# Optimization experiments

Hardware: AMD Instinct MI355X
Metric: run time of the kernel (lower is better)

Reference implementation:

```python
import jax, jax.numpy as jnp
import numpy as np

ALPHA = 1.0  # Student-t degrees of freedom (DEC default)


def setup_inputs() -> dict:
    key = jax.random.key(0)
    k1, k2 = jax.random.split(key)
    N, K, D = 32768, 1000, 1024
    h = jax.random.normal(k1, (N, D), dtype=jnp.float32)
    centroids = jax.random.normal(k2, (K, D), dtype=jnp.float32)
    return {"h": h, "centroids": centroids}


def reference(h, centroids):
    # squared pairwise L2 distance via the GEMM expansion:
    # ||h_i - mu_j||^2 = ||h_i||^2 + ||mu_j||^2 - 2 h_i . mu_j
    h_sq = jnp.sum(h * h, axis=1, keepdims=True)            # [N, 1]
    c_sq = jnp.sum(centroids * centroids, axis=1)           # [K]
    cross = jnp.einsum('nd,kd->nk', h, centroids)           # [N, K]
    d2 = jnp.maximum(h_sq + c_sq[None, :] - 2.0 * cross, 0.0)
    # Student-t kernel soft assignment (DEC):
    # q_ij = (1 + d2/alpha)^(-(alpha+1)/2) / sum_j'
    power = -(ALPHA + 1.0) / 2.0
    q = (1.0 + d2 / ALPHA) ** power                          # [N, K]
    q = q / jnp.sum(q, axis=1, keepdims=True)
    return q
```

## Files before the change

### kernel.cpp

```cpp
#include <hip/hip_runtime.h>


typedef unsigned short u16;
typedef __attribute__((ext_vector_type(8))) short bf16x8;
typedef __attribute__((ext_vector_type(4))) float f32x4;

#define N_ROWS 32768
#define K_CENT 1000
#define KP     1024
#define DDIM   1024

__device__ __forceinline__ u16 f2bf(float x) {
  unsigned u = __float_as_uint(x);
  u += 0x7fffu + ((u >> 16) & 1u);
  return (u16)(u >> 16);
}

__device__ __forceinline__ void gload_lds16(const u16* g, u16* s) {
  __builtin_amdgcn_global_load_lds((__attribute__((address_space(1))) void*)g,
                                   (__attribute__((address_space(3))) void*)s,
                                   16, 0, 0);
}


__global__ __launch_bounds__(256) void prep_h(const float* __restrict__ h,
                                              u16* __restrict__ hb,
                                              float* __restrict__ hsq,
                                              float* __restrict__ rowsum) {
  const int row = blockIdx.x;
  const int t = threadIdx.x;
  const float4 v = reinterpret_cast<const float4*>(h + (size_t)row * DDIM)[t];
  ushort4 b;
  b.x = f2bf(v.x); b.y = f2bf(v.y); b.z = f2bf(v.z); b.w = f2bf(v.w);
  reinterpret_cast<ushort4*>(hb + (size_t)row * DDIM)[t] = b;
  float ss = v.x * v.x + v.y * v.y + v.z * v.z + v.w * v.w;
#pragma unroll
  for (int m = 1; m < 64; m <<= 1) ss += __shfl_xor(ss, m);
  __shared__ float sbuf[4];
  if ((t & 63) == 0) sbuf[t >> 6] = ss;
  __syncthreads();
  if (t == 0) {
    hsq[row] = sbuf[0] + sbuf[1] + sbuf[2] + sbuf[3];
    rowsum[row] = 0.0f;
  }
}

__global__ __launch_bounds__(256) void prep_c(const float* __restrict__ c,
                                              u16* __restrict__ cb,
                                              float* __restrict__ csq) {
  const int row = blockIdx.x;
  const int t = threadIdx.x;
  if (row < K_CENT) {
    const float4 v = reinterpret_cast<const float4*>(c + (size_t)row * DDIM)[t];
    ushort4 b;
    b.x = f2bf(v.x); b.y = f2bf(v.y); b.z = f2bf(v.z); b.w = f2bf(v.w);
    reinterpret_cast<ushort4*>(cb + (size_t)row * DDIM)[t] = b;
    float ss = v.x * v.x + v.y * v.y + v.z * v.z + v.w * v.w;
#pragma unroll
    for (int m = 1; m < 64; m <<= 1) ss += __shfl_xor(ss, m);
    __shared__ float sbuf[4];
    if ((t & 63) == 0) sbuf[t >> 6] = ss;
    __syncthreads();
    if (t == 0) csq[row] = sbuf[0] + sbuf[1] + sbuf[2] + sbuf[3];
  } else {
    ushort4 z; z.x = z.y = z.z = z.w = 0;
    reinterpret_cast<ushort4*>(cb + (size_t)row * DDIM)[t] = z;
    if (t == 0) csq[row] = 1e30f;
  }
}


__device__ __forceinline__ void stage_tile(const u16* __restrict__ gA,
                                           const u16* __restrict__ gB,
                                           u16* sA, u16* sB,
                                           int w, int l, int k0) {
#pragma unroll
  for (int i = 0; i < 2; ++i) {
    const int c = w + i * 4;
    const int roff = c * 16 + (l >> 2);
    const int koff = (l & 3) * 8;
    const size_t go = (size_t)roff * DDIM + k0 + koff;
    gload_lds16(gA + go, sA + c * 512);
    gload_lds16(gB + go, sB + c * 512);
  }
}

__global__ __launch_bounds__(256) void gemm_q(const u16* __restrict__ hb,
                                              const u16* __restrict__ cb,
                                              const float* __restrict__ hsq,
                                              const float* __restrict__ csq,
                                              float* __restrict__ out,
                                              float* __restrict__ rowsum) {
  __shared__ u16 As[2][128 * 32];
  __shared__ u16 Bs[2][128 * 32];

  const int bid = blockIdx.x;
  const int swz = ((bid & 7) << 8) | (bid >> 3);
  const int bcol = swz & 7;
  const int brow = swz >> 3;

  const int t = threadIdx.x;
  const int w = t >> 6;
  const int l = t & 63;
  const int wr = w >> 1;
  const int wc = w & 1;

  const u16* gA = hb + (size_t)brow * 128 * DDIM;
  const u16* gB = cb + (size_t)bcol * 128 * DDIM;

  f32x4 acc[4][4] = {};

  stage_tile(gA, gB, &As[0][0], &Bs[0][0], w, l, 0);

  const int NT = DDIM / 32;
  for (int kt = 0; kt < NT; ++kt) {
    const int cur = kt & 1;
    __syncthreads();
    if (kt + 1 < NT)
      stage_tile(gA, gB, &As[cur ^ 1][0], &Bs[cur ^ 1][0], w, l, (kt + 1) * 32);

    bf16x8 aF[4], bF[4];
#pragma unroll
    for (int m = 0; m < 4; ++m) {
      aF[m] = *(const bf16x8*)&As[cur][(wr * 64 + m * 16 + (l & 15)) * 32 + (l >> 4) * 8];
      bF[m] = *(const bf16x8*)&Bs[cur][(wc * 64 + m * 16 + (l & 15)) * 32 + (l >> 4) * 8];
    }
#pragma unroll
    for (int m = 0; m < 4; ++m)
#pragma unroll
      for (int n = 0; n < 4; ++n)
        acc[m][n] = __builtin_amdgcn_mfma_f32_16x16x32_bf16(aF[m], bF[n], acc[m][n], 0, 0, 0);
  }

  const int gi0 = brow * 128 + wr * 64;
  const int gj0 = bcol * 128 + wc * 64;
  const int lr = (l >> 4) << 2;
  const int lc = l & 15;

#pragma unroll
  for (int m = 0; m < 4; ++m) {
    float hs[4];
#pragma unroll
    for (int r = 0; r < 4; ++r) hs[r] = hsq[gi0 + m * 16 + lr + r];
    float rs[4] = {0.f, 0.f, 0.f, 0.f};
#pragma unroll
    for (int n = 0; n < 4; ++n) {
      const int gj = gj0 + n * 16 + lc;
      const float cs = csq[gj];
#pragma unroll
      for (int r = 0; r < 4; ++r) {
        float d2 = hs[r] + cs - 2.0f * acc[m][n][r];
        d2 = fmaxf(d2, 0.0f);
        const float qv = 1.0f / (1.0f + d2);
        rs[r] += qv;
        if (gj < K_CENT)
          out[(size_t)(gi0 + m * 16 + lr + r) * K_CENT + gj] = qv;
      }
    }
#pragma unroll
    for (int r = 0; r < 4; ++r) {
      float v = rs[r];
      v += __shfl_xor(v, 1);
      v += __shfl_xor(v, 2);
      v += __shfl_xor(v, 4);
      v += __shfl_xor(v, 8);
      if (lc == 0) atomicAdd(&rowsum[gi0 + m * 16 + lr + r], v);
    }
  }
}


__global__ __launch_bounds__(256) void norm_k(float* __restrict__ out,
                                              const float* __restrict__ rowsum) {
  const int row = blockIdx.x;
  const int t = threadIdx.x;
  if (t < 250) {
    const float inv = 1.0f / rowsum[row];
    float4* p = reinterpret_cast<float4*>(out) + (size_t)row * 250 + t;
    float4 v = *p;
    v.x *= inv; v.y *= inv; v.z *= inv; v.w *= inv;
    *p = v;
  }
}


extern "C" void kernel_launch(void* const* d_in, const int* in_sizes, int n_in,
                              void* d_out, int out_size, void* d_ws, size_t ws_size,
                              hipStream_t stream) {
  const float* h   = (const float*)d_in[0];
  const float* cen = (const float*)d_in[1];
  float* out = (float*)d_out;
  char* ws = (char*)d_ws;

  u16*   cb     = (u16*)(ws);
  u16*   hb     = (u16*)(ws + 2097152);
  float* hsq    = (float*)(ws + 2097152 + 67108864);
  float* csq    = (float*)(ws + 2097152 + 67108864 + 131072);
  float* rowsum = (float*)(ws + 2097152 + 67108864 + 131072 + 4096);

  prep_c<<<KP, 256, 0, stream>>>(cen, cb, csq);
  prep_h<<<N_ROWS, 256, 0, stream>>>(h, hb, hsq, rowsum);
  gemm_q<<<(N_ROWS / 128) * (KP / 128), 256, 0, stream>>>(hb, cb, hsq, csq, out, rowsum);
  norm_k<<<N_ROWS, 256, 0, stream>>>(out, rowsum);
}
```

Measured before the change: 192.1 us.

## Enlarge GEMM tile to 256x256 with 4-stage LDS pipeline and swizzled layout

Moves the GEMM to 256x256 block tiles with 512 threads and 8 waves, each wave computing 128x64. A four-buffer LDS ring keeps three k-tiles in flight, with explicit vmcnt waits, barriers, and staging of the next tiles interleaved between MFMA groups. s_setprio is raised around the MFMA groups. An XOR swizzle on the LDS layout is meant to avoid bank conflicts. The goal is more data reuse per block and hiding of global-load latency. In exchange it uses much more LDS (128KB per block) and more accumulator registers, which lowers occupancy.

```diff
diff --git a/kernel.cpp b/kernel.cpp
--- a/kernel.cpp
+++ b/kernel.cpp
@@ -9,6 +9,7 @@
 #define K_CENT 1000
 #define KP     1024
 #define DDIM   1024
+#define NT     32
 
 __device__ __forceinline__ u16 f2bf(float x) {
   unsigned u = __float_as_uint(x);
@@ -70,75 +71,112 @@
 }
 
 
-__device__ __forceinline__ void stage_tile(const u16* __restrict__ gA,
-                                           const u16* __restrict__ gB,
-                                           u16* sA, u16* sB,
-                                           int w, int l, int k0) {
+__device__ __forceinline__ void stageA(const u16* __restrict__ gA, u16* sA,
+                                       int tid, int t) {
 #pragma unroll
   for (int i = 0; i < 2; ++i) {
-    const int c = w + i * 4;
-    const int roff = c * 16 + (l >> 2);
-    const int koff = (l & 3) * 8;
-    const size_t go = (size_t)roff * DDIM + k0 + koff;
-    gload_lds16(gA + go, sA + c * 512);
-    gload_lds16(gB + go, sB + c * 512);
-  }
-}
-
-__global__ __launch_bounds__(256) void gemm_q(const u16* __restrict__ hb,
-                                              const u16* __restrict__ cb,
-                                              const float* __restrict__ hsq,
-                                              const float* __restrict__ csq,
-                                              float* __restrict__ out,
-                                              float* __restrict__ rowsum) {
-  __shared__ u16 As[2][128 * 32];
-  __shared__ u16 Bs[2][128 * 32];
+    const int p = tid + i * 512;
+    const int g = p ^ ((p >> 3) & 7);
+    gload_lds16(gA + (size_t)(g >> 2) * DDIM + t * 32 + (g & 3) * 8,
+                sA + (((tid & ~63) + i * 512) << 3));
+  }
+}
+__device__ __forceinline__ void stageB(const u16* __restrict__ gB, u16* sB,
+                                       int tid, int t) {
+#pragma unroll
+  for (int i = 0; i < 2; ++i) {
+    const int p = tid + i * 512;
+    const int g = p ^ ((p >> 3) & 7);
+    gload_lds16(gB + (size_t)(g >> 2) * DDIM + t * 32 + (g & 3) * 8,
+                sB + (((tid & ~63) + i * 512) << 3));
+  }
+}
+
+__global__ __launch_bounds__(512, 2) void gemm_q(const u16* __restrict__ hb,
+                                                 const u16* __restrict__ cb,
+                                                 const float* __restrict__ hsq,
+                                                 const float* __restrict__ csq,
+                                                 float* __restrict__ out,
+                                                 float* __restrict__ rowsum) {
+  __shared__ u16 As[4][8192];
+  __shared__ u16 Bs[4][8192];
 
   const int bid = blockIdx.x;
-  const int swz = ((bid & 7) << 8) | (bid >> 3);
-  const int bcol = swz & 7;
-  const int brow = swz >> 3;
-
-  const int t = threadIdx.x;
-  const int w = t >> 6;
-  const int l = t & 63;
-  const int wr = w >> 1;
-  const int wc = w & 1;
-
-  const u16* gA = hb + (size_t)brow * 128 * DDIM;
-  const u16* gB = cb + (size_t)bcol * 128 * DDIM;
-
-  f32x4 acc[4][4] = {};
-
-  stage_tile(gA, gB, &As[0][0], &Bs[0][0], w, l, 0);
-
-  const int NT = DDIM / 32;
-  for (int kt = 0; kt < NT; ++kt) {
-    const int cur = kt & 1;
-    __syncthreads();
-    if (kt + 1 < NT)
-      stage_tile(gA, gB, &As[cur ^ 1][0], &Bs[cur ^ 1][0], w, l, (kt + 1) * 32);
-
-    bf16x8 aF[4], bF[4];
-#pragma unroll
-    for (int m = 0; m < 4; ++m) {
-      aF[m] = *(const bf16x8*)&As[cur][(wr * 64 + m * 16 + (l & 15)) * 32 + (l >> 4) * 8];
-      bF[m] = *(const bf16x8*)&Bs[cur][(wc * 64 + m * 16 + (l & 15)) * 32 + (l >> 4) * 8];
-    }
-#pragma unroll
-    for (int m = 0; m < 4; ++m)
-#pragma unroll
-      for (int n = 0; n < 4; ++n)
-        acc[m][n] = __builtin_amdgcn_mfma_f32_16x16x32_bf16(aF[m], bF[n], acc[m][n], 0, 0, 0);
-  }
-
-  const int gi0 = brow * 128 + wr * 64;
-  const int gj0 = bcol * 128 + wc * 64;
+  const int swz = ((bid & 7) << 6) | (bid >> 3);
+  const int bcol = swz & 3;
+  const int brow = swz >> 2;
+
+  const int tid = threadIdx.x;
+  const int w = tid >> 6;
+  const int l = tid & 63;
+  const int wm = w >> 2;
+  const int wn = w & 3;
+
+  const u16* gA = hb + (size_t)brow * 256 * DDIM;
+  const u16* gB = cb + (size_t)bcol * 256 * DDIM;
+
+  stageA(gA, As[0], tid, 0); stageB(gB, Bs[0], tid, 0);
+  stageA(gA, As[1], tid, 1); stageB(gB, Bs[1], tid, 1);
+  stageA(gA, As[2], tid, 2); stageB(gB, Bs[2], tid, 2);
+
+  int aOff[8], bOff[4];
+#pragma unroll
+  for (int m = 0; m < 8; ++m) {
+    const int row = wm * 128 + m * 16 + (l & 15);
+    const int g = (row << 2) | (l >> 4);
+    aOff[m] = (g ^ ((g >> 3) & 7)) << 3;
+  }
+#pragma unroll
+  for (int n = 0; n < 4; ++n) {
+    const int row = wn * 64 + n * 16 + (l & 15);
+    const int g = (row << 2) | (l >> 4);
+    bOff[n] = (g ^ ((g >> 3) & 7)) << 3;
+  }
+
+  f32x4 acc[8][4] = {};
+
+#define KTILE_BODY(T, VM)                                                      \
+  {                                                                            \
+    const int s_ = (T) & 3, ns_ = ((T) + 3) & 3;                               \
+    asm volatile("s_waitcnt vmcnt(" #VM ")" ::: "memory");                     \
+    __builtin_amdgcn_s_barrier();                                              \
+    __builtin_amdgcn_sched_barrier(0);                                         \
+    const u16* SA_ = As[s_]; const u16* SB_ = Bs[s_];                          \
+    bf16x8 aF[4], bF[4];                                                       \
+    _Pragma("unroll") for (int n = 0; n < 4; ++n)                              \
+        bF[n] = *(const bf16x8*)(SB_ + bOff[n]);                               \
+    _Pragma("unroll") for (int m = 0; m < 4; ++m)                              \
+        aF[m] = *(const bf16x8*)(SA_ + aOff[m]);                               \
+    if ((T) + 3 < NT) stageA(gA, As[ns_], tid, (T) + 3);                       \
+    __builtin_amdgcn_s_setprio(1);                                             \
+    _Pragma("unroll") for (int m = 0; m < 4; ++m)                              \
+      _Pragma("unroll") for (int n = 0; n < 4; ++n)                            \
+        acc[m][n] = __builtin_amdgcn_mfma_f32_16x16x32_bf16(aF[m], bF[n],      \
+                                                            acc[m][n], 0, 0, 0); \
+    __builtin_amdgcn_s_setprio(0);                                             \
+    _Pragma("unroll") for (int m = 0; m < 4; ++m)                              \
+        aF[m] = *(const bf16x8*)(SA_ + aOff[m + 4]);                           \
+    if ((T) + 3 < NT) stageB(gB, Bs[ns_], tid, (T) + 3);                       \
+    __builtin_amdgcn_s_setprio(1);                                             \
+    _Pragma("unroll") for (int m = 0; m < 4; ++m)                              \
+      _Pragma("unroll") for (int n = 0; n < 4; ++n)                            \
+        acc[m + 4][n] = __builtin_amdgcn_mfma_f32_16x16x32_bf16(aF[m], bF[n],  \
+                                                        acc[m + 4][n], 0, 0, 0); \
+    __builtin_amdgcn_s_setprio(0);                                             \
+  }
+
+  for (int t = 0; t < NT - 2; ++t) KTILE_BODY(t, 8)
+  KTILE_BODY(NT - 2, 4)
+  KTILE_BODY(NT - 1, 0)
+#undef KTILE_BODY
+
+  const int gi0 = brow * 256 + wm * 128;
+  const int gj0 = bcol * 256 + wn * 64;
   const int lr = (l >> 4) << 2;
   const int lc = l & 15;
 
 #pragma unroll
-  for (int m = 0; m < 4; ++m) {
+  for (int m = 0; m < 8; ++m) {
     float hs[4];
 #pragma unroll
     for (int r = 0; r < 4; ++r) hs[r] = hsq[gi0 + m * 16 + lr + r];
@@ -200,6 +238,6 @@
 
   prep_c<<<KP, 256, 0, stream>>>(cen, cb, csq);
   prep_h<<<N_ROWS, 256, 0, stream>>>(h, hb, hsq, rowsum);
-  gemm_q<<<(N_ROWS / 128) * (KP / 128), 256, 0, stream>>>(hb, cb, hsq, csq, out, rowsum);
+  gemm_q<<<(N_ROWS / 256) * (KP / 256), 512, 0, stream>>>(hb, cb, hsq, csq, out, rowsum);
   norm_k<<<N_ROWS, 256, 0, stream>>>(out, rowsum);
 }
```

After: 175.4 us. -8.7%, faster.

## Fuse row normalization into a full-row GEMM block with per-wave centroid slices

Applied to the files above, without the earlier changes.

Each block now computes a 64-row strip against all 1024 padded centroids: 8 waves each own 128 centroid columns. Row sums are reduced in LDS and the normalization is applied before the single store. This removes the separate normalize pass, the rowsum atomics and zeroing, and the extra read-modify-write of the 131 MB output. The A fragments are loaded directly from global into registers, and each wave stages its own swizzled B slice into LDS with manual vmcnt waits and no block barriers in the main loop. The trade-offs are a larger accumulator footprint (128 floats per lane) that may cut occupancy, and each block now rereads the entire centroid matrix.

```diff
diff --git a/kernel.cpp b/kernel.cpp
--- a/kernel.cpp
+++ b/kernel.cpp
@@ -9,6 +9,9 @@
 #define K_CENT 1000
 #define KP     1024
 #define DDIM   1024
+#define BM     64
+#define BK     32
+#define NT     32
 
 __device__ __forceinline__ u16 f2bf(float x) {
   unsigned u = __float_as_uint(x);
@@ -25,8 +28,7 @@
 
 __global__ __launch_bounds__(256) void prep_h(const float* __restrict__ h,
                                               u16* __restrict__ hb,
-                                              float* __restrict__ hsq,
-                                              float* __restrict__ rowsum) {
+                                              float* __restrict__ hsq) {
   const int row = blockIdx.x;
   const int t = threadIdx.x;
   const float4 v = reinterpret_cast<const float4*>(h + (size_t)row * DDIM)[t];
@@ -39,10 +41,7 @@
   __shared__ float sbuf[4];
   if ((t & 63) == 0) sbuf[t >> 6] = ss;
   __syncthreads();
-  if (t == 0) {
-    hsq[row] = sbuf[0] + sbuf[1] + sbuf[2] + sbuf[3];
-    rowsum[row] = 0.0f;
-  }
+  if (t == 0) hsq[row] = sbuf[0] + sbuf[1] + sbuf[2] + sbuf[3];
 }
 
 __global__ __launch_bounds__(256) void prep_c(const float* __restrict__ c,
@@ -70,117 +69,152 @@
 }
 
 
-__device__ __forceinline__ void stage_tile(const u16* __restrict__ gA,
-                                           const u16* __restrict__ gB,
-                                           u16* sA, u16* sB,
-                                           int w, int l, int k0) {
-#pragma unroll
-  for (int i = 0; i < 2; ++i) {
-    const int c = w + i * 4;
-    const int roff = c * 16 + (l >> 2);
-    const int koff = (l & 3) * 8;
-    const size_t go = (size_t)roff * DDIM + k0 + koff;
-    gload_lds16(gA + go, sA + c * 512);
-    gload_lds16(gB + go, sB + c * 512);
-  }
-}
-
-__global__ __launch_bounds__(256) void gemm_q(const u16* __restrict__ hb,
-                                              const u16* __restrict__ cb,
-                                              const float* __restrict__ hsq,
-                                              const float* __restrict__ csq,
-                                              float* __restrict__ out,
-                                              float* __restrict__ rowsum) {
-  __shared__ u16 As[2][128 * 32];
-  __shared__ u16 Bs[2][128 * 32];
-
-  const int bid = blockIdx.x;
-  const int swz = ((bid & 7) << 8) | (bid >> 3);
-  const int bcol = swz & 7;
-  const int brow = swz >> 3;
-
-  const int t = threadIdx.x;
-  const int w = t >> 6;
-  const int l = t & 63;
-  const int wr = w >> 1;
-  const int wc = w & 1;
-
-  const u16* gA = hb + (size_t)brow * 128 * DDIM;
-  const u16* gB = cb + (size_t)bcol * 128 * DDIM;
-
-  f32x4 acc[4][4] = {};
-
-  stage_tile(gA, gB, &As[0][0], &Bs[0][0], w, l, 0);
-
-  const int NT = DDIM / 32;
-  for (int kt = 0; kt < NT; ++kt) {
-    const int cur = kt & 1;
-    __syncthreads();
-    if (kt + 1 < NT)
-      stage_tile(gA, gB, &As[cur ^ 1][0], &Bs[cur ^ 1][0], w, l, (kt + 1) * 32);
-
-    bf16x8 aF[4], bF[4];
-#pragma unroll
-    for (int m = 0; m < 4; ++m) {
-      aF[m] = *(const bf16x8*)&As[cur][(wr * 64 + m * 16 + (l & 15)) * 32 + (l >> 4) * 8];
-      bF[m] = *(const bf16x8*)&Bs[cur][(wc * 64 + m * 16 + (l & 15)) * 32 + (l >> 4) * 8];
-    }
-#pragma unroll
-    for (int m = 0; m < 4; ++m)
-#pragma unroll
-      for (int n = 0; n < 4; ++n)
-        acc[m][n] = __builtin_amdgcn_mfma_f32_16x16x32_bf16(aF[m], bF[n], acc[m][n], 0, 0, 0);
-  }
-
-  const int gi0 = brow * 128 + wr * 64;
-  const int gj0 = bcol * 128 + wc * 64;
+__device__ __forceinline__ void stageB_w(const u16* __restrict__ gB, u16* sB,
+                                         int w, int l, int t) {
+#pragma unroll
+  for (int i = 0; i < 8; ++i) {
+    const int p = i * 64 + l;
+    const int g = p ^ ((p >> 3) & 7);
+    gload_lds16(gB + (size_t)(w * 128 + (g >> 2)) * DDIM + t * BK + (g & 3) * 8,
+                sB + ((i * 64) << 3));
+  }
+}
+
+__device__ __forceinline__ void loadA(const u16* __restrict__ gA, bf16x8* fA,
+                                      int l, int t) {
+  const int r = l & 15;
+  const int kc = t * BK + (l >> 4) * 8;
+#pragma unroll
+  for (int m = 0; m < 4; ++m)
+    fA[m] = *(const bf16x8*)(gA + (size_t)(m * 16 + r) * DDIM + kc);
+}
+
+__global__ __launch_bounds__(512) void gemm_row(const u16* __restrict__ hb,
+                                                const u16* __restrict__ cb,
+                                                const float* __restrict__ hsq,
+                                                const float* __restrict__ csq,
+                                                float* __restrict__ out) {
+  __shared__ u16 Bs[8][2][128 * BK];
+
+  const int brow = blockIdx.x;
+  const int tid = threadIdx.x;
+  const int w = tid >> 6;
+  const int l = tid & 63;
+
+  const u16* gA = hb + (size_t)brow * BM * DDIM;
+  const u16* gB = cb;
+  u16* myB0 = &Bs[w][0][0];
+  u16* myB1 = &Bs[w][1][0];
+
+  int bOff0;
+  {
+    const int g = ((l & 15) << 2) | (l >> 4);
+    bOff0 = (g ^ ((g >> 3) & 7)) << 3;
+  }
+
+  f32x4 acc[4][8] = {};
+  bf16x8 fA0[4], fA1[4];
+
+  stageB_w(gB, myB0, w, l, 0);
+  loadA(gA, fA0, l, 0);
+
+#define MFMA_HALF(FA, SB, NB)                                                  \
+  {                                                                            \
+    bf16x8 fB[4];                                                              \
+    _Pragma("unroll") for (int n = 0; n < 4; ++n)                              \
+        fB[n] = *(const bf16x8*)((SB) + bOff0 + ((NB) * 4 + n) * 512);         \
+    _Pragma("unroll") for (int m = 0; m < 4; ++m)                              \
+      _Pragma("unroll") for (int n = 0; n < 4; ++n)                            \
+        acc[m][(NB) * 4 + n] = __builtin_amdgcn_mfma_f32_16x16x32_bf16(        \
+            (FA)[m], fB[n], acc[m][(NB) * 4 + n], 0, 0, 0);                    \
+  }
+
+#define ITER(T, FAc, FAn, MYBc, MYBn, ISSUE, VMSTR)                            \
+  {                                                                            \
+    if (ISSUE) { stageB_w(gB, MYBn, w, l, (T) + 1); loadA(gA, FAn, l, (T) + 1); } \
+    asm volatile("s_waitcnt vmcnt(" VMSTR ")" ::: "memory");                   \
+    __builtin_amdgcn_s_setprio(1);                                             \
+    MFMA_HALF(FAc, MYBc, 0)                                                    \
+    MFMA_HALF(FAc, MYBc, 1)                                                    \
+    __builtin_amdgcn_s_setprio(0);                                             \
+  }
+
+#pragma unroll 1
+  for (int t = 0; t < NT - 2; t += 2) {
+    ITER(t,     fA0, fA1, myB0, myB1, true, "12")
+    ITER(t + 1, fA1, fA0, myB1, myB0, true, "12")
+  }
+  ITER(NT - 2, fA0, fA1, myB0, myB1, true,  "12")
+  ITER(NT - 1, fA1, fA0, myB1, myB0, false, "0")
+#undef ITER
+#undef MFMA_HALF
+
+  __builtin_amdgcn_s_barrier();
+  float* part = (float*)&Bs[0][0][0];
+  float* inv  = part + 512;
+
   const int lr = (l >> 4) << 2;
   const int lc = l & 15;
 
+  float rsv[4][4];
 #pragma unroll
   for (int m = 0; m < 4; ++m) {
     float hs[4];
 #pragma unroll
-    for (int r = 0; r < 4; ++r) hs[r] = hsq[gi0 + m * 16 + lr + r];
-    float rs[4] = {0.f, 0.f, 0.f, 0.f};
-#pragma unroll
-    for (int n = 0; n < 4; ++n) {
-      const int gj = gj0 + n * 16 + lc;
-      const float cs = csq[gj];
+    for (int r = 0; r < 4; ++r) hs[r] = hsq[brow * BM + m * 16 + lr + r];
+#pragma unroll
+    for (int r = 0; r < 4; ++r) rsv[m][r] = 0.f;
+#pragma unroll
+    for (int n = 0; n < 8; ++n) {
+      const float cs = csq[w * 128 + n * 16 + lc];
 #pragma unroll
       for (int r = 0; r < 4; ++r) {
         float d2 = hs[r] + cs - 2.0f * acc[m][n][r];
         d2 = fmaxf(d2, 0.0f);
         const float qv = 1.0f / (1.0f + d2);
-        rs[r] += qv;
-        if (gj < K_CENT)
-          out[(size_t)(gi0 + m * 16 + lr + r) * K_CENT + gj] = qv;
+        acc[m][n][r] = qv;
+        rsv[m][r] += qv;
       }
     }
+  }
+#pragma unroll
+  for (int m = 0; m < 4; ++m)
 #pragma unroll
     for (int r = 0; r < 4; ++r) {
-      float v = rs[r];
+      float v = rsv[m][r];
       v += __shfl_xor(v, 1);
       v += __shfl_xor(v, 2);
       v += __shfl_xor(v, 4);
       v += __shfl_xor(v, 8);
-      if (lc == 0) atomicAdd(&rowsum[gi0 + m * 16 + lr + r], v);
+      if (lc == 0) part[w * 64 + m * 16 + lr + r] = v;
     }
-  }
-}
-
-
-__global__ __launch_bounds__(256) void norm_k(float* __restrict__ out,
-                                              const float* __restrict__ rowsum) {
-  const int row = blockIdx.x;
-  const int t = threadIdx.x;
-  if (t < 250) {
-    const float inv = 1.0f / rowsum[row];
-    float4* p = reinterpret_cast<float4*>(out) + (size_t)row * 250 + t;
-    float4 v = *p;
-    v.x *= inv; v.y *= inv; v.z *= inv; v.w *= inv;
-    *p = v;
-  }
+  __syncthreads();
+  if (tid < 64) {
+    float s = 0.f;
+#pragma unroll
+    for (int w2 = 0; w2 < 8; ++w2) s += part[w2 * 64 + tid];
+    inv[tid] = 1.0f / s;
+  }
+  __syncthreads();
+
+  float iv[4][4];
+#pragma unroll
+  for (int m = 0; m < 4; ++m)
+#pragma unroll
+    for (int r = 0; r < 4; ++r) iv[m][r] = inv[m * 16 + lr + r];
+
+#pragma unroll
+  for (int m = 0; m < 4; ++m)
+#pragma unroll
+    for (int n = 0; n < 8; ++n) {
+      const int col = w * 128 + n * 16 + lc;
+      if (col < K_CENT) {
+#pragma unroll
+        for (int r = 0; r < 4; ++r)
+          out[(size_t)(brow * BM + m * 16 + lr + r) * K_CENT + col] =
+              acc[m][n][r] * iv[m][r];
+      }
+    }
 }
 
 
@@ -192,14 +226,12 @@
   float* out = (float*)d_out;
   char* ws = (char*)d_ws;
 
-  u16*   cb     = (u16*)(ws);
-  u16*   hb     = (u16*)(ws + 2097152);
-  float* hsq    = (float*)(ws + 2097152 + 67108864);
-  float* csq    = (float*)(ws + 2097152 + 67108864 + 131072);
-  float* rowsum = (float*)(ws + 2097152 + 67108864 + 131072 + 4096);
+  u16*   cb  = (u16*)(ws);
+  u16*   hb  = (u16*)(ws + 2097152);
+  float* hsq = (float*)(ws + 2097152 + 67108864);
+  float* csq = (float*)(ws + 2097152 + 67108864 + 131072);
 
   prep_c<<<KP, 256, 0, stream>>>(cen, cb, csq);
-  prep_h<<<N_ROWS, 256, 0, stream>>>(h, hb, hsq, rowsum);
-  gemm_q<<<(N_ROWS / 128) * (KP / 128), 256, 0, stream>>>(hb, cb, hsq, csq, out, rowsum);
-  norm_k<<<N_ROWS, 256, 0, stream>>>(out, rowsum);
-}
+  prep_h<<<N_ROWS, 256, 0, stream>>>(h, hb, hsq);
+  gemm_row<<<N_ROWS / BM, 512, 0, stream>>>(hb, cb, hsq, csq, out);
+}
```

New measurement: 181.0 us. -5.8%, faster.

## Register-prefetch GEMM tiles two steps ahead into an XOR-swizzled single LDS buffer

Applied to the files above, without the earlier changes.

Replaces the direct global-to-LDS loads and the double-buffered LDS tiles with register-staged loads fetched two k-tiles ahead. Each tile is written into a single LDS buffer whose 16-byte chunks are XOR-swizzled, so the MFMA fragment reads avoid bank conflicts. Raw s_barrier calls fence the compute and write phases. This is meant to hide global latency better and speed up LDS reads, at the cost of more registers and an extra barrier per k-step.

```diff
diff --git a/kernel.cpp b/kernel.cpp
--- a/kernel.cpp
+++ b/kernel.cpp
@@ -9,17 +9,12 @@
 #define K_CENT 1000
 #define KP     1024
 #define DDIM   1024
+#define NT     32
 
 __device__ __forceinline__ u16 f2bf(float x) {
   unsigned u = __float_as_uint(x);
   u += 0x7fffu + ((u >> 16) & 1u);
   return (u16)(u >> 16);
-}
-
-__device__ __forceinline__ void gload_lds16(const u16* g, u16* s) {
-  __builtin_amdgcn_global_load_lds((__attribute__((address_space(1))) void*)g,
-                                   (__attribute__((address_space(3))) void*)s,
-                                   16, 0, 0);
 }
 
 
@@ -70,29 +65,13 @@
 }
 
 
-__device__ __forceinline__ void stage_tile(const u16* __restrict__ gA,
-                                           const u16* __restrict__ gB,
-                                           u16* sA, u16* sB,
-                                           int w, int l, int k0) {
-#pragma unroll
-  for (int i = 0; i < 2; ++i) {
-    const int c = w + i * 4;
-    const int roff = c * 16 + (l >> 2);
-    const int koff = (l & 3) * 8;
-    const size_t go = (size_t)roff * DDIM + k0 + koff;
-    gload_lds16(gA + go, sA + c * 512);
-    gload_lds16(gB + go, sB + c * 512);
-  }
-}
-
 __global__ __launch_bounds__(256) void gemm_q(const u16* __restrict__ hb,
                                               const u16* __restrict__ cb,
                                               const float* __restrict__ hsq,
                                               const float* __restrict__ csq,
                                               float* __restrict__ out,
                                               float* __restrict__ rowsum) {
-  __shared__ u16 As[2][128 * 32];
-  __shared__ u16 Bs[2][128 * 32];
+  __shared__ u16 SM[8192];
 
   const int bid = blockIdx.x;
   const int swz = ((bid & 7) << 8) | (bid >> 3);
@@ -108,29 +87,70 @@
   const u16* gA = hb + (size_t)brow * 128 * DDIM;
   const u16* gB = cb + (size_t)bcol * 128 * DDIM;
 
+  const int g0 = t, g1 = t + 256;
+  const int p0 = g0 ^ ((g0 >> 3) & 7);
+  const int p1 = g1 ^ ((g1 >> 3) & 7);
+  const size_t ga0 = (size_t)(g0 >> 2) * DDIM + (g0 & 3) * 8;
+  const size_t ga1 = (size_t)(g1 >> 2) * DDIM + (g1 & 3) * 8;
+
+#define GLOAD(RA, RB, T)                                                       \
+  {                                                                            \
+    const int kk = (T) * 32;                                                   \
+    RA[0] = *(const bf16x8*)(gA + ga0 + kk);                                   \
+    RA[1] = *(const bf16x8*)(gA + ga1 + kk);                                   \
+    RB[0] = *(const bf16x8*)(gB + ga0 + kk);                                   \
+    RB[1] = *(const bf16x8*)(gB + ga1 + kk);                                   \
+  }
+#define SWRITE(RA, RB)                                                         \
+  {                                                                            \
+    *(bf16x8*)&SM[p0 << 3] = RA[0];                                            \
+    *(bf16x8*)&SM[p1 << 3] = RA[1];                                            \
+    *(bf16x8*)&SM[4096 + (p0 << 3)] = RB[0];                                   \
+    *(bf16x8*)&SM[4096 + (p1 << 3)] = RB[1];                                   \
+  }
+
+  const int hi = l >> 4;
+  int aOff[4], bOff[4];
+#pragma unroll
+  for (int m = 0; m < 4; ++m) {
+    const int ga = ((wr * 64 + m * 16 + (l & 15)) << 2) | hi;
+    const int gb = ((wc * 64 + m * 16 + (l & 15)) << 2) | hi;
+    aOff[m] = (ga ^ ((ga >> 3) & 7)) << 3;
+    bOff[m] = 4096 + ((gb ^ ((gb >> 3) & 7)) << 3);
+  }
+
   f32x4 acc[4][4] = {};
-
-  stage_tile(gA, gB, &As[0][0], &Bs[0][0], w, l, 0);
-
-  const int NT = DDIM / 32;
-  for (int kt = 0; kt < NT; ++kt) {
-    const int cur = kt & 1;
-    __syncthreads();
-    if (kt + 1 < NT)
-      stage_tile(gA, gB, &As[cur ^ 1][0], &Bs[cur ^ 1][0], w, l, (kt + 1) * 32);
-
-    bf16x8 aF[4], bF[4];
-#pragma unroll
-    for (int m = 0; m < 4; ++m) {
-      aF[m] = *(const bf16x8*)&As[cur][(wr * 64 + m * 16 + (l & 15)) * 32 + (l >> 4) * 8];
-      bF[m] = *(const bf16x8*)&Bs[cur][(wc * 64 + m * 16 + (l & 15)) * 32 + (l >> 4) * 8];
-    }
-#pragma unroll
-    for (int m = 0; m < 4; ++m)
-#pragma unroll
-      for (int n = 0; n < 4; ++n)
-        acc[m][n] = __builtin_amdgcn_mfma_f32_16x16x32_bf16(aF[m], bF[n], acc[m][n], 0, 0, 0);
-  }
+  bf16x8 pAa[2], pBa[2], pAb[2], pBb[2];
+
+  GLOAD(pAa, pBa, 0)
+  GLOAD(pAb, pBb, 1)
+  SWRITE(pAa, pBa)
+  __syncthreads();
+
+#define ITER(T, SNa, SNb, SFa, SFb)                                            \
+  {                                                                            \
+    if ((T) + 2 < NT) GLOAD(SFa, SFb, (T) + 2)                                 \
+    bf16x8 aF[4], bF[4];                                                       \
+    _Pragma("unroll") for (int m = 0; m < 4; ++m)                              \
+        aF[m] = *(const bf16x8*)&SM[aOff[m]];                                  \
+    _Pragma("unroll") for (int n = 0; n < 4; ++n)                              \
+        bF[n] = *(const bf16x8*)&SM[bOff[n]];                                  \
+    _Pragma("unroll") for (int m = 0; m < 4; ++m)                              \
+      _Pragma("unroll") for (int n = 0; n < 4; ++n)                            \
+        acc[m][n] = __builtin_amdgcn_mfma_f32_16x16x32_bf16(aF[m], bF[n],      \
+                                                            acc[m][n], 0, 0, 0); \
+    __builtin_amdgcn_s_barrier();                                              \
+    if ((T) + 1 < NT) { SWRITE(SNa, SNb) __builtin_amdgcn_s_barrier(); }       \
+  }
+
+#pragma unroll 1
+  for (int kt = 0; kt < NT; kt += 2) {
+    ITER(kt,     pAb, pBb, pAa, pBa)
+    ITER(kt + 1, pAa, pBa, pAb, pBb)
+  }
+#undef ITER
+#undef GLOAD
+#undef SWRITE
 
   const int gi0 = brow * 128 + wr * 64;
   const int gj0 = bcol * 128 + wc * 64;
```

After: 202.3 us. 1.05x slower.
